# Optimization experiments

Measured on AMD Instinct MI355X. Metric: run time of the kernel, lower is better.

## Reference

```python
import jax, jax.numpy as jnp
import numpy as np

POS_FACTOR = 1.0
CLASS_FACTOR = 1.0
EDGE_FACTOR = 1.0
LOG_CLAMP = -100.0  # torch BCELoss clamps log terms at -100


def setup_inputs() -> dict:
    key = jax.random.key(0)
    ks = jax.random.split(key, 8)
    B, N, E, C = 64, 54, 54, 5
    G = (B, 20, 128, 128)
    pred_nodes = jax.random.normal(ks[0], (B, 3 + C), dtype=jnp.float32)
    # sigmoid-like probabilities in (0,1)
    pred_edges = jax.random.uniform(ks[1], (B, E), dtype=jnp.float32, minval=1e-4, maxval=1.0 - 1e-4)
    pred_dist = jax.random.normal(ks[2], G, dtype=jnp.float32)
    pos_r = jax.random.uniform(ks[3], (B, N, 3), dtype=jnp.float32) * 10.0  # atom positions in angstroms
    cls_r = jax.random.randint(ks[4], (B, N, 1), 0, C).astype(jnp.float32)  # class index stored as float col 3
    ref_nodes = jnp.concatenate([pos_r, cls_r], axis=-1)
    ref_edges = jax.random.bernoulli(ks[5], 0.3, (B, N, E)).astype(jnp.float32)
    ref_terminate = jax.random.randint(ks[6], (B,), 0, 2, dtype=jnp.int32)
    ref_dist = jax.random.normal(ks[7], G, dtype=jnp.float32)
    return {
        'pred_nodes': pred_nodes, 'pred_edges': pred_edges, 'pred_dist': pred_dist,
        'ref_nodes': ref_nodes, 'ref_edges': ref_edges, 'ref_terminate': ref_terminate,
        'ref_dist': ref_dist,
    }


def reference(pred_nodes, pred_edges, pred_dist, ref_nodes, ref_edges, ref_terminate, ref_dist):
    # Grid MSE per batch item: mean over (C,H,W)
    mse_pos = jnp.mean((pred_dist - ref_dist) ** 2, axis=(1, 2, 3))  # [B]

    # Nearest reference atom to predicted position (per item)
    pos_p = pred_nodes[:, None, :3]            # [B,1,3]
    pos_r = ref_nodes[:, :, :3]                # [B,N,3]
    d2 = jnp.sum((pos_r - pos_p) ** 2, -1)     # [B,N]
    min_inds = jnp.argmin(d2, axis=1)          # [B]

    # Masked cross-entropy on node class logits vs matched reference class
    logits = pred_nodes[:, 3:]                                         # [B,C]
    cls_r = ref_nodes[:, :, 3].astype(jnp.int32)                       # [B,N]
    tgt = jnp.take_along_axis(cls_r, min_inds[:, None], axis=1)[:, 0]  # [B]
    ce = jax.nn.logsumexp(logits, axis=-1) - jnp.take_along_axis(
        logits, tgt[:, None], axis=1)[:, 0]                            # [B]
    active = (ref_terminate == 0).astype(pred_nodes.dtype)             # [B]
    nll_class = active * ce

    # Masked BCE on edge probabilities vs matched reference edge row
    sel_edges = jnp.take_along_axis(ref_edges, min_inds[:, None, None], axis=1)[:, 0, :]  # [B,E]
    log_p = jnp.maximum(jnp.log(pred_edges), LOG_CLAMP)
    log_1mp = jnp.maximum(jnp.log1p(-pred_edges), LOG_CLAMP)
    bce = -jnp.mean(sel_edges * log_p + (1.0 - sel_edges) * log_1mp, axis=1)  # [B]
    nll_edge = active * bce
    nll_edge = jnp.where(jnp.isnan(nll_edge), 0.0, nll_edge)

    loss = (POS_FACTOR * jnp.mean(mse_pos)
            + CLASS_FACTOR * jnp.mean(nll_class)
            + EDGE_FACTOR * jnp.mean(nll_edge))
    return loss, min_inds
```

## Files before the change

### kernel.cpp

```cpp
#include <hip/hip_runtime.h>
#include <math.h>

#define NPART 2048
#define MSE_THREADS 256
#define MSE_UNROLL 10
#define B 64
#define N 54
#define E 54
#define C 5
#define LOG_CLAMP (-100.0f)

__global__ __launch_bounds__(MSE_THREADS) void k_main(const float* __restrict__ pred_dist,
                                                      const float* __restrict__ ref_dist,
                                                      const float* __restrict__ pred_nodes,
                                                      const float* __restrict__ pred_edges,
                                                      const float* __restrict__ ref_nodes,
                                                      const float* __restrict__ ref_edges,
                                                      const int* __restrict__ ref_term,
                                                      float* __restrict__ part,
                                                      float* __restrict__ nll,
                                                      float* __restrict__ out,
                                                      int n4) {
    if (blockIdx.x < NPART) {
        const float4* __restrict__ p4 = (const float4*)pred_dist;
        const float4* __restrict__ r4 = (const float4*)ref_dist;
        const int stride = NPART * MSE_THREADS;
        int idx = blockIdx.x * MSE_THREADS + threadIdx.x;
        float acc = 0.0f;

        if (n4 == stride * MSE_UNROLL) {
            float4 a[MSE_UNROLL], b[MSE_UNROLL];
            #pragma unroll
            for (int u = 0; u < MSE_UNROLL; u++) a[u] = p4[idx + u * stride];
            #pragma unroll
            for (int u = 0; u < MSE_UNROLL; u++) b[u] = r4[idx + u * stride];
            #pragma unroll
            for (int u = 0; u < MSE_UNROLL; u++) {
                float d0 = a[u].x - b[u].x, d1 = a[u].y - b[u].y;
                float d2 = a[u].z - b[u].z, d3 = a[u].w - b[u].w;
                acc = fmaf(d0, d0, acc);
                acc = fmaf(d1, d1, acc);
                acc = fmaf(d2, d2, acc);
                acc = fmaf(d3, d3, acc);
            }
        } else {
            for (int i = idx; i < n4; i += stride) {
                float4 a = p4[i];
                float4 b = r4[i];
                float d0 = a.x - b.x, d1 = a.y - b.y, d2 = a.z - b.z, d3 = a.w - b.w;
                acc = fmaf(d0, d0, acc);
                acc = fmaf(d1, d1, acc);
                acc = fmaf(d2, d2, acc);
                acc = fmaf(d3, d3, acc);
            }
        }

        #pragma unroll
        for (int off = 32; off > 0; off >>= 1) acc += __shfl_down(acc, off, 64);
        __shared__ float s[MSE_THREADS / 64];
        int lane = threadIdx.x & 63;
        int w = threadIdx.x >> 6;
        if (lane == 0) s[w] = acc;
        __syncthreads();
        if (threadIdx.x == 0) {
            float t = 0.0f;
            #pragma unroll
            for (int i = 0; i < MSE_THREADS / 64; i++) t += s[i];
            part[blockIdx.x] = t;
        }
    } else {
        int b = blockIdx.x - NPART;
        int t = threadIdx.x;
        if (t >= 64) return;
        const float* pn = pred_nodes + b * (3 + C);
        float px = pn[0], py = pn[1], pz = pn[2];

        float d2 = 1e30f;
        int mi = t;
        if (t < N) {
            const float* rn = ref_nodes + ((long)b * N + t) * 4;
            float dx = rn[0] - px, dy = rn[1] - py, dz = rn[2] - pz;
            d2 = dx * dx + dy * dy + dz * dz;
        }
        #pragma unroll
        for (int off = 32; off > 0; off >>= 1) {
            float od = __shfl_down(d2, off, 64);
            int oi = __shfl_down(mi, off, 64);
            if (od < d2 || (od == d2 && oi < mi)) { d2 = od; mi = oi; }
        }
        mi = __shfl(mi, 0, 64);

        int tgt = (int)ref_nodes[((long)b * N + mi) * 4 + 3];
        const float* logits = pn + 3;
        float m = logits[0];
        #pragma unroll
        for (int c = 1; c < C; c++) m = fmaxf(m, logits[c]);
        float se = 0.0f;
        #pragma unroll
        for (int c = 0; c < C; c++) se += __expf(logits[c] - m);
        float ce = logf(se) + m - logits[tgt];

        float term = 0.0f;
        if (t < E) {
            float sel = ref_edges[((long)b * N + mi) * E + t];
            float p = pred_edges[b * E + t];
            float lp = fmaxf(logf(p), LOG_CLAMP);
            float l1mp = fmaxf(log1pf(-p), LOG_CLAMP);
            term = -(sel * lp + (1.0f - sel) * l1mp);
        }
        #pragma unroll
        for (int off = 32; off > 0; off >>= 1) term += __shfl_down(term, off, 64);

        if (t == 0) {
            float active = (ref_term[b] == 0) ? 1.0f : 0.0f;
            float ne = active * (term / (float)E);
            if (isnan(ne)) ne = 0.0f;
            nll[b] = active * ce + ne;
            out[1 + b] = (float)mi;
        }
    }
}

__global__ __launch_bounds__(256) void k_final(const float* __restrict__ part,
                                               const float* __restrict__ nll,
                                               float* __restrict__ out,
                                               float inv_total) {
    int t = threadIdx.x;
    int lane = t & 63;
    int w = t >> 6;
    float acc = 0.0f;
    for (int i = t; i < NPART; i += 256) acc += part[i];
    float nacc = (t < B) ? nll[t] : 0.0f;
    #pragma unroll
    for (int off = 32; off > 0; off >>= 1) {
        acc += __shfl_down(acc, off, 64);
        nacc += __shfl_down(nacc, off, 64);
    }
    __shared__ float s_p[4], s_n[4];
    if (lane == 0) { s_p[w] = acc; s_n[w] = nacc; }
    __syncthreads();
    if (t == 0) {
        float mse = (s_p[0] + s_p[1] + s_p[2] + s_p[3]) * inv_total;
        float ns = s_n[0] + s_n[1] + s_n[2] + s_n[3];
        out[0] = mse + ns * (1.0f / (float)B);
    }
}

extern "C" void kernel_launch(void* const* d_in, const int* in_sizes, int n_in,
                              void* d_out, int out_size, void* d_ws, size_t ws_size,
                              hipStream_t stream) {
    const float* pred_nodes = (const float*)d_in[0];
    const float* pred_edges = (const float*)d_in[1];
    const float* pred_dist  = (const float*)d_in[2];
    const float* ref_nodes  = (const float*)d_in[3];
    const float* ref_edges  = (const float*)d_in[4];
    const int*   ref_term   = (const int*)d_in[5];
    const float* ref_dist   = (const float*)d_in[6];

    float* out  = (float*)d_out;
    float* part = (float*)d_ws;
    float* nll  = part + NPART;

    int n_dist = in_sizes[2];
    int n4 = n_dist / 4;

    k_main<<<NPART + B, MSE_THREADS, 0, stream>>>(pred_dist, ref_dist, pred_nodes,
                                                  pred_edges, ref_nodes, ref_edges,
                                                  ref_term, part, nll, out, n4);
    k_final<<<1, 256, 0, stream>>>(part, nll, out, 1.0f / (float)n_dist);
}
```

Baseline: 36.99 us.

## Fuse final reduction into main kernel via last-block atomic counter

Result: slower. 99.10 us (+167.9%).

```diff
diff --git a/kernel.cpp b/kernel.cpp
--- a/kernel.cpp
+++ b/kernel.cpp
@@ -8,6 +8,7 @@
 #define N 54
 #define E 54
 #define C 5
+#define TOTAL_BLOCKS (NPART + B)
 #define LOG_CLAMP (-100.0f)
 
 __global__ __launch_bounds__(MSE_THREADS) void k_main(const float* __restrict__ pred_dist,
@@ -17,15 +18,18 @@
                                                       const float* __restrict__ ref_nodes,
                                                       const float* __restrict__ ref_edges,
                                                       const int* __restrict__ ref_term,
+                                                      unsigned int* __restrict__ cnt,
                                                       float* __restrict__ part,
                                                       float* __restrict__ nll,
                                                       float* __restrict__ out,
-                                                      int n4) {
+                                                      int n4, float inv_total) {
+    const int t = threadIdx.x;
+
     if (blockIdx.x < NPART) {
         const float4* __restrict__ p4 = (const float4*)pred_dist;
         const float4* __restrict__ r4 = (const float4*)ref_dist;
         const int stride = NPART * MSE_THREADS;
-        int idx = blockIdx.x * MSE_THREADS + threadIdx.x;
+        int idx = blockIdx.x * MSE_THREADS + t;
         float acc = 0.0f;
 
         if (n4 == stride * MSE_UNROLL) {
@@ -34,6 +38,7 @@
             for (int u = 0; u < MSE_UNROLL; u++) a[u] = p4[idx + u * stride];
             #pragma unroll
             for (int u = 0; u < MSE_UNROLL; u++) b[u] = r4[idx + u * stride];
+            __builtin_amdgcn_sched_barrier(0);
             #pragma unroll
             for (int u = 0; u < MSE_UNROLL; u++) {
                 float d0 = a[u].x - b[u].x, d1 = a[u].y - b[u].y;
@@ -58,20 +63,18 @@
         #pragma unroll
         for (int off = 32; off > 0; off >>= 1) acc += __shfl_down(acc, off, 64);
         __shared__ float s[MSE_THREADS / 64];
-        int lane = threadIdx.x & 63;
-        int w = threadIdx.x >> 6;
+        int lane = t & 63;
+        int w = t >> 6;
         if (lane == 0) s[w] = acc;
         __syncthreads();
-        if (threadIdx.x == 0) {
-            float t = 0.0f;
+        if (t == 0) {
+            float v = 0.0f;
             #pragma unroll
-            for (int i = 0; i < MSE_THREADS / 64; i++) t += s[i];
-            part[blockIdx.x] = t;
+            for (int i = 0; i < MSE_THREADS / 64; i++) v += s[i];
+            part[blockIdx.x] = v;
         }
-    } else {
+    } else if (t < 64) {
         int b = blockIdx.x - NPART;
-        int t = threadIdx.x;
-        if (t >= 64) return;
         const float* pn = pred_nodes + b * (3 + C);
         float px = pn[0], py = pn[1], pz = pn[2];
 
@@ -119,30 +122,39 @@
             out[1 + b] = (float)mi;
         }
     }
-}
 
-__global__ __launch_bounds__(256) void k_final(const float* __restrict__ part,
-                                               const float* __restrict__ nll,
-                                               float* __restrict__ out,
-                                               float inv_total) {
-    int t = threadIdx.x;
-    int lane = t & 63;
-    int w = t >> 6;
-    float acc = 0.0f;
-    for (int i = t; i < NPART; i += 256) acc += part[i];
-    float nacc = (t < B) ? nll[t] : 0.0f;
-    #pragma unroll
-    for (int off = 32; off > 0; off >>= 1) {
-        acc += __shfl_down(acc, off, 64);
-        nacc += __shfl_down(nacc, off, 64);
+    __shared__ int s_last;
+    if (t == 0) {
+        __threadfence();
+        unsigned int old = atomicAdd(cnt, 1u);
+        s_last = (old == (unsigned int)(TOTAL_BLOCKS - 1)) ? 1 : 0;
     }
-    __shared__ float s_p[4], s_n[4];
-    if (lane == 0) { s_p[w] = acc; s_n[w] = nacc; }
     __syncthreads();
-    if (t == 0) {
-        float mse = (s_p[0] + s_p[1] + s_p[2] + s_p[3]) * inv_total;
-        float ns = s_n[0] + s_n[1] + s_n[2] + s_n[3];
-        out[0] = mse + ns * (1.0f / (float)B);
+    if (s_last) {
+        __threadfence();
+        const float4* part4 = (const float4*)part;
+        float acc = 0.0f;
+        #pragma unroll
+        for (int r = 0; r < NPART / 4 / MSE_THREADS; r++) {
+            float4 v = part4[t + r * MSE_THREADS];
+            acc += (v.x + v.y) + (v.z + v.w);
+        }
+        float nacc = (t < B) ? nll[t] : 0.0f;
+        #pragma unroll
+        for (int off = 32; off > 0; off >>= 1) {
+            acc += __shfl_down(acc, off, 64);
+            nacc += __shfl_down(nacc, off, 64);
+        }
+        __shared__ float s_p[4], s_n[4];
+        int lane = t & 63;
+        int w = t >> 6;
+        if (lane == 0) { s_p[w] = acc; s_n[w] = nacc; }
+        __syncthreads();
+        if (t == 0) {
+            float mse = (s_p[0] + s_p[1] + s_p[2] + s_p[3]) * inv_total;
+            float ns = s_n[0] + s_n[1] + s_n[2] + s_n[3];
+            out[0] = mse + ns * (1.0f / (float)B);
+        }
     }
 }
 
@@ -157,15 +169,17 @@
     const int*   ref_term   = (const int*)d_in[5];
     const float* ref_dist   = (const float*)d_in[6];
 
-    float* out  = (float*)d_out;
-    float* part = (float*)d_ws;
+    float* out = (float*)d_out;
+    unsigned int* cnt = (unsigned int*)d_ws;
+    float* part = (float*)d_ws + 4;
     float* nll  = part + NPART;
 
     int n_dist = in_sizes[2];
     int n4 = n_dist / 4;
 
-    k_main<<<NPART + B, MSE_THREADS, 0, stream>>>(pred_dist, ref_dist, pred_nodes,
-                                                  pred_edges, ref_nodes, ref_edges,
-                                                  ref_term, part, nll, out, n4);
-    k_final<<<1, 256, 0, stream>>>(part, nll, out, 1.0f / (float)n_dist);
+    hipMemsetAsync(d_ws, 0, 4, stream);
+    k_main<<<TOTAL_BLOCKS, MSE_THREADS, 0, stream>>>(pred_dist, ref_dist, pred_nodes,
+                                                     pred_edges, ref_nodes, ref_edges,
+                                                     ref_term, cnt, part, nll, out,
+                                                     n4, 1.0f / (float)n_dist);
 }
```
